# Kernel optimization log

Hardware: AMD Instinct MI355X
Metric: run time of the kernel (lower is better)

The kernel has to match this reference:

```python
import jax, jax.numpy as jnp
import numpy as np

B, L, D, H, K = 4, 2048, 1024, 16, 256
DH = D // H
SCALE = DH ** -0.5


def setup_inputs() -> dict:
    key = jax.random.key(0)
    ks = jax.random.split(key, 8)
    std = 1.0 / np.sqrt(D)
    pstd = 1.0 / np.sqrt(K)  # init_ uses last dim of (seq_len, k) tensor
    return {
        "x": jax.random.normal(ks[0], (B, L, D), dtype=jnp.float32),
        "Wq": jax.random.uniform(ks[1], (D, D), jnp.float32, -std, std),
        "Wk": jax.random.uniform(ks[2], (D, D), jnp.float32, -std, std),
        "Wv": jax.random.uniform(ks[3], (D, D), jnp.float32, -std, std),
        "proj_k": jax.random.uniform(ks[4], (L, K), jnp.float32, -pstd, pstd),
        "proj_v": jax.random.uniform(ks[5], (L, K), jnp.float32, -pstd, pstd),
        "Wo": jax.random.uniform(ks[6], (D, D), jnp.float32, -std, std),
        "bo": jax.random.uniform(ks[7], (D,), jnp.float32, -std, std),
    }


def reference(x, Wq, Wk, Wv, proj_k, proj_v, Wo, bo):
    b, l, d = x.shape
    q = x @ Wq.T                                   # [B,L,D]
    keys = jnp.einsum("bnd,nk->bkd", x @ Wk.T, proj_k)   # [B,K,D]
    vals = jnp.einsum("bnd,nk->bkd", x @ Wv.T, proj_v)   # [B,K,D]
    # faithful to original: plain reshape (B,h,L,d_h), NOT transpose-split
    q = q.reshape(b, H, l, DH)
    k = keys.reshape(b, K, H, DH).transpose(0, 2, 1, 3)  # [B,H,K,DH]
    v = vals.reshape(b, K, H, DH).transpose(0, 2, 1, 3)  # [B,H,K,DH]
    attn = jax.nn.softmax(jnp.einsum("bhld,bhkd->bhlk", q, k) * SCALE, axis=-1)
    out = jnp.einsum("bhlk,bhkd->bhld", attn, v)
    out = out.transpose(0, 2, 1, 3).reshape(b, l, d)
    return out @ Wo.T + bo
```

## Files before the change

### kernel.cpp

```cpp
#include <hip/hip_runtime.h>


typedef __attribute__((ext_vector_type(8))) short short8;
typedef __attribute__((ext_vector_type(4))) short short4_t;
typedef __attribute__((ext_vector_type(4))) float facc;

#define B_    4
#define L_    2048
#define D_    1024
#define H_    16
#define KP    256
#define DH_   64
#define SCALE_ 0.125f
#define PTS   76

__device__ __forceinline__ short f2b(float f) {
  unsigned u = __float_as_uint(f);
  unsigned r = (u + 0x7fffu + ((u >> 16) & 1u)) >> 16;
  return (short)r;
}

__device__ __forceinline__ void load16_to_lds(const short* gp, short* lp) {
  __builtin_amdgcn_global_load_lds(
      (const __attribute__((address_space(1))) void*)gp,
      (__attribute__((address_space(3))) void*)lp, 16, 0, 0);
}

__global__ __launch_bounds__(256) void prepX(
    const float* __restrict__ x,  const float* __restrict__ pk,
    const float* __restrict__ pv, const float* __restrict__ w0,
    const float* __restrict__ w1, const float* __restrict__ w2,
    const float* __restrict__ w3, short* __restrict__ xb,
    short* __restrict__ xTb, short* __restrict__ projT,
    short* __restrict__ Wb)
{
  const int z = blockIdx.z, tid = threadIdx.x;
  if (z >= 6) {
    const int bid  = blockIdx.y * 32 + blockIdx.x;
    const int widx = (z - 6) * 2 + (bid >> 10);
    const float* s = (widx == 0) ? w0 : (widx == 1) ? w1 : (widx == 2) ? w2 : w3;
    const int i = ((bid & 1023) * 256 + tid) * 4;
    float4 f = *(const float4*)(s + i);
    short4_t v; v[0] = f2b(f.x); v[1] = f2b(f.y); v[2] = f2b(f.z); v[3] = f2b(f.w);
    *(short4_t*)(Wb + (size_t)widx * 1048576 + i) = v;
    return;
  }

  __shared__ float tl[32][37];
  const int row = tid >> 3, c4 = tid & 7;

  if (z < 4) {
    const int b = z, l0 = blockIdx.y * 32, d0 = blockIdx.x * 32;
    const float* s = x + (size_t)b * L_ * D_;
    float4 f = *(const float4*)(s + (size_t)(l0 + row) * D_ + d0 + c4 * 4);
    short4_t v; v[0] = f2b(f.x); v[1] = f2b(f.y); v[2] = f2b(f.z); v[3] = f2b(f.w);
    *(short4_t*)(xb + (size_t)b * L_ * D_ + (size_t)(l0 + row) * D_ + d0 + c4 * 4) = v;
    tl[row][c4 * 4 + 0] = f.x; tl[row][c4 * 4 + 1] = f.y;
    tl[row][c4 * 4 + 2] = f.z; tl[row][c4 * 4 + 3] = f.w;
    __syncthreads();
    short4_t t;
#pragma unroll
    for (int j = 0; j < 4; j++) t[j] = f2b(tl[c4 * 4 + j][row]);
    *(short4_t*)(xTb + (size_t)b * D_ * L_ + (size_t)(d0 + row) * L_ + l0 + c4 * 4) = t;
  } else {
    if (blockIdx.x >= 8) return;
    const int sel = z - 4, l0 = blockIdx.y * 32, k0 = blockIdx.x * 32;
    const float* s = sel ? pv : pk;
    float4 f = *(const float4*)(s + (size_t)(l0 + row) * KP + k0 + c4 * 4);
    tl[row][c4 * 4 + 0] = f.x; tl[row][c4 * 4 + 1] = f.y;
    tl[row][c4 * 4 + 2] = f.z; tl[row][c4 * 4 + 3] = f.w;
    __syncthreads();
    short4_t t;
#pragma unroll
    for (int j = 0; j < 4; j++) t[j] = f2b(tl[c4 * 4 + j][row]);
    *(short4_t*)(projT + (size_t)sel * (KP * L_) + (size_t)(k0 + row) * L_ + l0 + c4 * 4) = t;
  }
}

__global__ __launch_bounds__(512, 2) void gemm8p(
    const short* __restrict__ Am, const short* __restrict__ Bm,
    const float* __restrict__ bias, float* __restrict__ C32,
    short* __restrict__ Cb, int M, int N, int K)
{
  extern __shared__ __attribute__((aligned(16))) short smem[];
  constexpr int BUF  = 24576;
  constexpr int BOFF = 16384;

  const int t = threadIdx.x, lane = t & 63, w = t >> 6;
  const int lm = lane & 15, g = lane >> 4;
  const int bm = blockIdx.x * 4 + (blockIdx.y >> 3);
  const int bn = blockIdx.y & 7;
  const int m0 = bm * 256, n0 = bn * 128;
  const int wm = (w & 3) * 64, wn = (w >> 2) * 64;

  const int srow = lane >> 2;
  const int sslot = lane & 3;

  facc acc[4][4];
  const facc fz = {0.f, 0.f, 0.f, 0.f};
#pragma unroll
  for (int i = 0; i < 4; i++)
#pragma unroll
    for (int j = 0; j < 4; j++) acc[i][j] = fz;

  auto stageA = [&](int kt, int buf, int rnd) {
    const int task = rnd * 8 + w;
    const int c = task >> 4, grp = task & 15;
    const int row = grp * 16 + srow;
    const int slot = sslot ^ ((row >> 1) & 3);
    load16_to_lds(Am + (size_t)(m0 + row) * K + kt * 64 + c * 32 + slot * 8,
                  smem + buf * BUF + c * 8192 + grp * 512);
  };
  auto stageB = [&](int kt, int buf, int rnd) {
    const int task = rnd * 8 + w;
    const int c = task >> 3, grp = task & 7;
    const int row = grp * 16 + srow;
    const int slot = sslot ^ ((row >> 1) & 3);
    load16_to_lds(Bm + (size_t)(n0 + row) * K + kt * 64 + c * 32 + slot * 8,
                  smem + buf * BUF + BOFF + c * 4096 + grp * 512);
  };

#pragma unroll
  for (int r = 0; r < 4; r++) stageA(0, 0, r);
#pragma unroll
  for (int r = 0; r < 2; r++) stageB(0, 0, r);
#pragma unroll
  for (int r = 0; r < 4; r++) stageA(1, 1, r);
#pragma unroll
  for (int r = 0; r < 2; r++) stageB(1, 1, r);
  asm volatile("s_waitcnt vmcnt(6)" ::: "memory");
  __builtin_amdgcn_sched_barrier(0);
  __builtin_amdgcn_s_barrier();

  const int T = K >> 6;
  int p = 0;
  for (int kt = 0; kt < T; kt++) {
    const int q = (p == 0) ? 2 : p - 1;
    const bool pf = (kt + 2 < T);

#pragma unroll
    for (int c = 0; c < 2; c++) {
      short8 af[4], bf[4];
      const int abase = p * BUF + c * 8192;
      const int bbase = p * BUF + BOFF + c * 4096;
#pragma unroll
      for (int mt = 0; mt < 4; mt++) {
        const int row = wm + 16 * mt + lm;
        af[mt] = *(const short8*)(smem + abase + row * 32 + ((g ^ ((row >> 1) & 3)) * 8));
      }
#pragma unroll
      for (int nt = 0; nt < 4; nt++) {
        const int row = wn + 16 * nt + lm;
        bf[nt] = *(const short8*)(smem + bbase + row * 32 + ((g ^ ((row >> 1) & 3)) * 8));
      }
      if (pf) {
        if (c == 0) { stageA(kt + 2, q, 0); stageA(kt + 2, q, 1); stageB(kt + 2, q, 0); }
        else        { stageA(kt + 2, q, 2); stageA(kt + 2, q, 3); stageB(kt + 2, q, 1); }
      }
      __builtin_amdgcn_s_barrier();
      __builtin_amdgcn_s_setprio(1);
#pragma unroll
      for (int mt = 0; mt < 4; mt++)
#pragma unroll
        for (int nt = 0; nt < 4; nt++)
          acc[mt][nt] = __builtin_amdgcn_mfma_f32_16x16x32_bf16(af[mt], bf[nt], acc[mt][nt], 0, 0, 0);
      __builtin_amdgcn_s_setprio(0);
      if (c == 0) __builtin_amdgcn_s_barrier();
    }

    if (pf) {
      asm volatile("s_waitcnt vmcnt(6)" ::: "memory");
      __builtin_amdgcn_sched_barrier(0);
    } else if (kt + 1 < T) {
      asm volatile("s_waitcnt vmcnt(0)" ::: "memory");
      __builtin_amdgcn_sched_barrier(0);
    }
    __builtin_amdgcn_s_barrier();
    p = (p == 2) ? 0 : p + 1;
  }

#pragma unroll
  for (int mt = 0; mt < 4; mt++)
#pragma unroll
    for (int r = 0; r < 4; r++) {
      const int row = m0 + wm + 16 * mt + 4 * g + r;
#pragma unroll
      for (int nt = 0; nt < 4; nt++) {
        const int col = n0 + wn + 16 * nt + lm;
        float v = acc[mt][nt][r];
        if (bias) v += bias[col];
        if (C32) C32[(size_t)row * N + col] = v;
        if (Cb)  Cb[(size_t)row * N + col] = f2b(v);
      }
    }
}

__global__ __launch_bounds__(256) void gemm_p64x128(
    const short* __restrict__ Am, const short* __restrict__ Bm,
    const float* __restrict__ bias, float* __restrict__ C32,
    short* __restrict__ Cb, short* __restrict__ CbT, int M, int N, int K,
    long aHi, long aLo, long bHi, long bLo, long cHi, long cLo, int zDiv)
{
  __shared__ __attribute__((aligned(16))) short smem[3 * 12288];
  const int t = threadIdx.x, lane = t & 63, w = t >> 6;
  const int lm = lane & 15, g = lane >> 4;
  const int z = blockIdx.z, zhi = z / zDiv, zlo = z % zDiv;
  const int m0 = blockIdx.y * 64, n0 = blockIdx.x * 128;
  const int wm = (w & 1) * 32, wn = (w >> 1) * 64;

  const short* Ab = Am + zhi * aHi + zlo * aLo;
  const short* Bp = Bm + zhi * bHi + zlo * bLo;

  const int srow = lane >> 2;
  const int sslot = lane & 3;

  facc acc[2][4];
  const facc fz = {0.f, 0.f, 0.f, 0.f};
#pragma unroll
  for (int i = 0; i < 2; i++)
#pragma unroll
    for (int j = 0; j < 4; j++) acc[i][j] = fz;

  auto stage_h = [&](int kt, int buf, int c) {
    const int arow = w * 16 + srow;
    const int aslot = sslot ^ ((arow >> 1) & 3);
    load16_to_lds(Ab + (size_t)(m0 + arow) * K + kt * 64 + c * 32 + aslot * 8,
                  smem + buf * 12288 + c * 2048 + w * 512);
#pragma unroll
    for (int jj = 0; jj < 2; jj++) {
      const int j = w + jj * 4;
      const int brow = j * 16 + srow;
      const int bslot = sslot ^ ((brow >> 1) & 3);
      load16_to_lds(Bp + (size_t)(n0 + brow) * K + kt * 64 + c * 32 + bslot * 8,
                    smem + buf * 12288 + 4096 + c * 4096 + j * 512);
    }
  };

  stage_h(0, 0, 0); stage_h(0, 0, 1);
  stage_h(1, 1, 0); stage_h(1, 1, 1);
  asm volatile("s_waitcnt vmcnt(6)" ::: "memory");
  __builtin_amdgcn_sched_barrier(0);
  __builtin_amdgcn_s_barrier();

  const int T = K >> 6;
  int p = 0;
  for (int kt = 0; kt < T; kt++) {
    const int q = (p == 0) ? 2 : p - 1;
    const bool pf = (kt + 2 < T);

#pragma unroll
    for (int c = 0; c < 2; c++) {
      short8 af[2], bf[4];
      const int abase = p * 12288 + c * 2048;
      const int bbase = p * 12288 + 4096 + c * 4096;
#pragma unroll
      for (int mt = 0; mt < 2; mt++) {
        const int row = wm + 16 * mt + lm;
        af[mt] = *(const short8*)(smem + abase + row * 32 + ((g ^ ((row >> 1) & 3)) * 8));
      }
#pragma unroll
      for (int nt = 0; nt < 4; nt++) {
        const int row = wn + 16 * nt + lm;
        bf[nt] = *(const short8*)(smem + bbase + row * 32 + ((g ^ ((row >> 1) & 3)) * 8));
      }
      if (pf) stage_h(kt + 2, q, c);
      __builtin_amdgcn_s_setprio(1);
#pragma unroll
      for (int mt = 0; mt < 2; mt++)
#pragma unroll
        for (int nt = 0; nt < 4; nt++)
          acc[mt][nt] = __builtin_amdgcn_mfma_f32_16x16x32_bf16(af[mt], bf[nt], acc[mt][nt], 0, 0, 0);
      __builtin_amdgcn_s_setprio(0);
    }

    if (pf) {
      asm volatile("s_waitcnt vmcnt(6)" ::: "memory");
      __builtin_amdgcn_sched_barrier(0);
    } else if (kt + 1 < T) {
      asm volatile("s_waitcnt vmcnt(0)" ::: "memory");
      __builtin_amdgcn_sched_barrier(0);
    }
    __builtin_amdgcn_s_barrier();
    p = (p == 2) ? 0 : p + 1;
  }

  if (CbT && zhi == 1) {
#pragma unroll
    for (int mt = 0; mt < 2; mt++) {
      const int rb = m0 + wm + 16 * mt + 4 * g;
      const size_t bb = (size_t)(rb >> 8) * (16 * 64 * 256);
      const int kp = rb & 255;
#pragma unroll
      for (int nt = 0; nt < 4; nt++) {
        const int col = n0 + wn + 16 * nt + lm;
        short4_t o4;
#pragma unroll
        for (int r = 0; r < 4; r++) o4[r] = f2b(acc[mt][nt][r]);
        *(short4_t*)(CbT + bb + (size_t)col * KP + kp) = o4;
      }
    }
    return;
  }

  const long cz = zhi * cHi + zlo * cLo;
#pragma unroll
  for (int mt = 0; mt < 2; mt++)
#pragma unroll
    for (int r = 0; r < 4; r++) {
      const int row = m0 + wm + 16 * mt + 4 * g + r;
#pragma unroll
      for (int nt = 0; nt < 4; nt++) {
        const int col = n0 + wn + 16 * nt + lm;
        float v = acc[mt][nt][r];
        if (bias) v += bias[col];
        if (C32) C32[cz + (size_t)row * N + col] = v;
        if (Cb)  Cb[cz + (size_t)row * N + col] = f2b(v);
      }
    }
}

__global__ __launch_bounds__(256) void attn_mfma(
    const short* __restrict__ xqb, const short* __restrict__ keysb,
    const short* __restrict__ vTb, short* __restrict__ out2b)
{
  __shared__ __attribute__((aligned(16))) short Pt[4][32 * PTS];

  const int t = threadIdx.x, lane = t & 63, w = t >> 6;
  const int lm = lane & 15, g = lane >> 4;
  const int b = blockIdx.z, h = blockIdx.y;
  const int l0w = blockIdx.x * 128 + w * 32;

  short8 aq[2][2];
#pragma unroll
  for (int mt = 0; mt < 2; mt++) {
    const int l = l0w + 16 * mt + lm;
    const short* qrow = xqb + ((size_t)b * L_ + h * 128 + (l >> 4)) * D_ + (l & 15) * DH_;
#pragma unroll
    for (int ks = 0; ks < 2; ks++)
      aq[mt][ks] = *(const short8*)(qrow + ks * 32 + g * 8);
  }

  facc accO[2][4];
  const facc fz = {0.f, 0.f, 0.f, 0.f};
#pragma unroll
  for (int mt = 0; mt < 2; mt++)
#pragma unroll
    for (int dt = 0; dt < 4; dt++) accO[mt][dt] = fz;
  float lrow[2][4];
#pragma unroll
  for (int mt = 0; mt < 2; mt++)
#pragma unroll
    for (int r = 0; r < 4; r++) lrow[mt][r] = 0.f;

  const short* Kb = keysb + (size_t)b * KP * D_ + h * DH_;
  const short* Vb = vTb + ((size_t)b * H_ + h) * DH_ * KP;

  for (int c = 0; c < 4; c++) {
    facc S[2][4];
#pragma unroll
    for (int mt = 0; mt < 2; mt++)
#pragma unroll
      for (int nt = 0; nt < 4; nt++) S[mt][nt] = fz;
#pragma unroll
    for (int ks = 0; ks < 2; ks++) {
      short8 bk[4];
#pragma unroll
      for (int nt = 0; nt < 4; nt++)
        bk[nt] = *(const short8*)(Kb + (size_t)(c * 64 + 16 * nt + lm) * D_ + ks * 32 + g * 8);
#pragma unroll
      for (int mt = 0; mt < 2; mt++)
#pragma unroll
        for (int nt = 0; nt < 4; nt++)
          S[mt][nt] = __builtin_amdgcn_mfma_f32_16x16x32_bf16(aq[mt][ks], bk[nt], S[mt][nt], 0, 0, 0);
    }

#pragma unroll
    for (int mt = 0; mt < 2; mt++)
#pragma unroll
      for (int r = 0; r < 4; r++) {
        float ps = 0.f;
        const int prow = (16 * mt + 4 * g + r) * PTS;
#pragma unroll
        for (int nt = 0; nt < 4; nt++) {
          const float p = __expf(S[mt][nt][r] * SCALE_);
          ps += p;
          Pt[w][prow + 16 * nt + lm] = f2b(p);
        }
        lrow[mt][r] += ps;
      }

#pragma unroll
    for (int ks = 0; ks < 2; ks++) {
      short8 ap[2], bv[4];
#pragma unroll
      for (int mt = 0; mt < 2; mt++)
        ap[mt] = *(const short8*)(&Pt[w][(16 * mt + lm) * PTS + ks * 32 + g * 8]);
#pragma unroll
      for (int dt = 0; dt < 4; dt++)
        bv[dt] = *(const short8*)(Vb + (size_t)(16 * dt + lm) * KP + c * 64 + ks * 32 + g * 8);
#pragma unroll
      for (int mt = 0; mt < 2; mt++)
#pragma unroll
        for (int dt = 0; dt < 4; dt++)
          accO[mt][dt] = __builtin_amdgcn_mfma_f32_16x16x32_bf16(ap[mt], bv[dt], accO[mt][dt], 0, 0, 0);
    }
  }

#pragma unroll
  for (int mt = 0; mt < 2; mt++)
#pragma unroll
    for (int r = 0; r < 4; r++) {
      float ls = lrow[mt][r];
      ls += __shfl_xor(ls, 1);
      ls += __shfl_xor(ls, 2);
      ls += __shfl_xor(ls, 4);
      ls += __shfl_xor(ls, 8);
      const float inv = 1.0f / ls;
      const int l = l0w + 16 * mt + 4 * g + r;
#pragma unroll
      for (int dt = 0; dt < 4; dt++)
        out2b[((size_t)b * L_ + l) * D_ + h * DH_ + 16 * dt + lm] = f2b(accO[mt][dt][r] * inv);
    }
}

extern "C" void kernel_launch(void* const* d_in, const int* in_sizes, int n_in,
                              void* d_out, int out_size, void* d_ws, size_t ws_size,
                              hipStream_t stream)
{
  const float* x      = (const float*)d_in[0];
  const float* Wq     = (const float*)d_in[1];
  const float* Wk     = (const float*)d_in[2];
  const float* Wv     = (const float*)d_in[3];
  const float* proj_k = (const float*)d_in[4];
  const float* proj_v = (const float*)d_in[5];
  const float* Wo     = (const float*)d_in[6];
  const float* bo     = (const float*)d_in[7];
  float* out = (float*)d_out;

  short* ws     = (short*)d_ws;
  short* xqb    = ws;
  short* xTb    = xqb    + 8388608;
  short* xb     = xTb    + 8388608;
  short* out2b  = xb;
  short* Wqb    = xb     + 8388608;
  short* Wkb    = Wqb    + 1048576;
  short* Wvb    = Wkb    + 1048576;
  short* Wob    = Wvb    + 1048576;
  short* projTk = Wob    + 1048576;
  short* projTv = projTk + 524288;
  short* xk2b   = projTv + 524288;
  short* xv2b   = xk2b   + 1048576;
  short* keysb  = xv2b   + 1048576;
  short* valsb  = keysb  + 1048576;
  short* vT     = valsb  + 1048576;
  (void)Wkb; (void)Wvb; (void)projTv; (void)xv2b; (void)valsb;

  static bool attr_set = false;
  if (!attr_set) {
    (void)hipFuncSetAttribute(reinterpret_cast<const void*>(gemm8p),
                              hipFuncAttributeMaxDynamicSharedMemorySize, 147456);
    attr_set = true;
  }

  prepX<<<dim3(32, 64, 8), 256, 0, stream>>>(
      x, proj_k, proj_v, Wq, Wk, Wv, Wo, xb, xTb, projTk, Wqb);

  gemm8p<<<dim3(8, 32, 1), 512, 147456, stream>>>(
      xb, Wqb, nullptr, nullptr, xqb, 8192, 1024, 1024);

  gemm_p64x128<<<dim3(8, 4, 8), 256, 0, stream>>>(
      projTk, xTb, nullptr, nullptr, xk2b, nullptr, 256, 1024, 2048,
      524288, 0, 0, (long)D_ * L_, 1048576, 262144, 4);

  gemm_p64x128<<<dim3(8, 16, 2), 256, 0, stream>>>(
      xk2b, Wkb, nullptr, nullptr, keysb, vT, 1024, 1024, 1024,
      1048576, 0, 1048576, 0, 0, 0, 1);

  attn_mfma<<<dim3(16, 16, 4), 256, 0, stream>>>(xqb, keysb, vT, out2b);

  gemm8p<<<dim3(8, 32, 1), 512, 147456, stream>>>(
      out2b, Wob, bo, out, nullptr, 8192, 1024, 1024);
}
```

Before: 234.6 us.

## Stage K/V chunks in double-buffered LDS with register prefetch in attention kernel

The attention kernel now cooperatively loads each 64-key chunk of K and V into padded, double-buffered shared memory. Each of the four waves then reads its MFMA operands from LDS instead of issuing its own redundant global loads. The next chunk is prefetched into registers and written to the alternate buffer while the current chunk is computed, with a block barrier per iteration. This trades redundant global/L2 traffic for extra LDS use, a barrier per chunk, and higher register pressure.

```diff
diff --git a/kernel.cpp b/kernel.cpp
--- a/kernel.cpp
+++ b/kernel.cpp
@@ -323,6 +323,8 @@
     const short* __restrict__ xqb, const short* __restrict__ keysb,
     const short* __restrict__ vTb, short* __restrict__ out2b)
 {
+  __shared__ __attribute__((aligned(16))) short Kt[2][64 * 72];
+  __shared__ __attribute__((aligned(16))) short Vt[2][64 * 72];
   __shared__ __attribute__((aligned(16))) short Pt[4][32 * PTS];
 
   const int t = threadIdx.x, lane = t & 63, w = t >> 6;
@@ -355,7 +357,29 @@
   const short* Kb = keysb + (size_t)b * KP * D_ + h * DH_;
   const short* Vb = vTb + ((size_t)b * H_ + h) * DH_ * KP;
 
+  const int srow = t >> 3, sch = (t & 7) * 8;
+
+#pragma unroll
+  for (int i = 0; i < 2; i++) {
+    const int row = srow + 32 * i;
+    *(short8*)(&Kt[0][row * 72 + sch]) = *(const short8*)(Kb + (size_t)row * D_ + sch);
+    *(short8*)(&Vt[0][row * 72 + sch]) = *(const short8*)(Vb + (size_t)row * KP + sch);
+  }
+  __syncthreads();
+
   for (int c = 0; c < 4; c++) {
+    const int bi = c & 1;
+
+    short8 kr[2], vr[2];
+    if (c < 3) {
+#pragma unroll
+      for (int i = 0; i < 2; i++) {
+        const int row = srow + 32 * i;
+        kr[i] = *(const short8*)(Kb + (size_t)((c + 1) * 64 + row) * D_ + sch);
+        vr[i] = *(const short8*)(Vb + (size_t)row * KP + (c + 1) * 64 + sch);
+      }
+    }
+
     facc S[2][4];
 #pragma unroll
     for (int mt = 0; mt < 2; mt++)
@@ -366,12 +390,21 @@
       short8 bk[4];
 #pragma unroll
       for (int nt = 0; nt < 4; nt++)
-        bk[nt] = *(const short8*)(Kb + (size_t)(c * 64 + 16 * nt + lm) * D_ + ks * 32 + g * 8);
+        bk[nt] = *(const short8*)(&Kt[bi][(16 * nt + lm) * 72 + ks * 32 + g * 8]);
 #pragma unroll
       for (int mt = 0; mt < 2; mt++)
 #pragma unroll
         for (int nt = 0; nt < 4; nt++)
           S[mt][nt] = __builtin_amdgcn_mfma_f32_16x16x32_bf16(aq[mt][ks], bk[nt], S[mt][nt], 0, 0, 0);
+    }
+
+    if (c < 3) {
+#pragma unroll
+      for (int i = 0; i < 2; i++) {
+        const int row = srow + 32 * i;
+        *(short8*)(&Kt[bi ^ 1][row * 72 + sch]) = kr[i];
+        *(short8*)(&Vt[bi ^ 1][row * 72 + sch]) = vr[i];
+      }
     }
 
 #pragma unroll
@@ -397,13 +430,14 @@
         ap[mt] = *(const short8*)(&Pt[w][(16 * mt + lm) * PTS + ks * 32 + g * 8]);
 #pragma unroll
       for (int dt = 0; dt < 4; dt++)
-        bv[dt] = *(const short8*)(Vb + (size_t)(16 * dt + lm) * KP + c * 64 + ks * 32 + g * 8);
+        bv[dt] = *(const short8*)(&Vt[bi][(16 * dt + lm) * 72 + ks * 32 + g * 8]);
 #pragma unroll
       for (int mt = 0; mt < 2; mt++)
 #pragma unroll
         for (int dt = 0; dt < 4; dt++)
           accO[mt][dt] = __builtin_amdgcn_mfma_f32_16x16x32_bf16(ap[mt], bv[dt], accO[mt][dt], 0, 0, 0);
     }
+    __syncthreads();
   }
 
 #pragma unroll
```

Result: faster. 217.1 us (-7.5%).
